# Performance work log

Measured on AMD Instinct MI355X. Metric: run time of the kernel, lower is better.

## Reference

```python
import jax, jax.numpy as jnp
import numpy as np
from math import sqrt

B, IN_C, OUT_C, H, W, WDIM, K = 16, 512, 512, 64, 64, 512, 3
EPS = 1e-8
LRELU_SLOPE = 0.2


def setup_inputs() -> dict:
    key = jax.random.key(0)
    ks = jax.random.split(key, 5)
    return {
        "x": jax.random.normal(ks[0], (B, IN_C, H, W), dtype=jnp.float32),
        "w": jax.random.normal(ks[1], (B, WDIM), dtype=jnp.float32),
        "noise": jax.random.normal(ks[2], (B, 1, H, W), dtype=jnp.float32),
        "linear_w": jax.random.normal(ks[3], (IN_C, WDIM), dtype=jnp.float32),
        "linear_b": jnp.ones((IN_C,), dtype=jnp.float32),
        "conv_w": jax.random.normal(ks[4], (OUT_C, IN_C, K, K), dtype=jnp.float32),
        "scale_noise": jnp.zeros((OUT_C,), dtype=jnp.float32),
        "bias": jnp.zeros((OUT_C,), dtype=jnp.float32),
    }


def reference(x, w, noise, linear_w, linear_b, conv_w, scale_noise, bias):
    # EqualizerStraights: equalized-lr linear, scale = 1/sqrt(w_dim)
    s = w @ (linear_w * (1.0 / sqrt(WDIM))).T + linear_b  # [b, in_c]
    # Weight_Demod: equalized conv weight, scale = 1/sqrt(in_c*k*k)
    base_w = conv_w * (1.0 / sqrt(IN_C * K * K))  # [out, in, k, k]
    weights = base_w[None] * s[:, None, :, None, None]  # [b, out, in, k, k]
    sigma_inv = jax.lax.rsqrt(
        jnp.sum(weights * weights, axis=(2, 3, 4), keepdims=True) + EPS)
    weights = weights * sigma_inv

    def conv1(xi, wi):  # xi [in,h,w], wi [out,in,k,k]
        return jax.lax.conv_general_dilated(
            xi[None], wi, window_strides=(1, 1), padding="SAME",
            dimension_numbers=("NCHW", "OIHW", "NCHW"))[0]

    y = jax.vmap(conv1)(x, weights)  # [b, out, h, w]
    y = y + scale_noise[None, :, None, None] * noise
    return jax.nn.leaky_relu(y + bias[None, :, None, None], negative_slope=LRELU_SLOPE)
```

## Files before the change

kernel.cpp:

```cpp
#include <hip/hip_runtime.h>
#include <hip/hip_bf16.h>
#include <stdint.h>

typedef __bf16 bf16_t;
typedef __bf16 bf16x8 __attribute__((ext_vector_type(8)));
typedef short short8 __attribute__((ext_vector_type(8)));
typedef float f32x4 __attribute__((ext_vector_type(4)));

#define RS512  0.044194173824159216f
#define RS4608 0.014731391274719739f

__global__ void k_style(const float* __restrict__ w, const float* __restrict__ lw,
                        const float* __restrict__ lb, float* __restrict__ s) {
  int b = blockIdx.y;
  int c = blockIdx.x * 256 + threadIdx.x;
  const float4* wr = (const float4*)(w + b * 512);
  const float4* lr = (const float4*)(lw + (size_t)c * 512);
  float acc = 0.f;
#pragma unroll 4
  for (int d = 0; d < 128; ++d) {
    float4 a = wr[d], q = lr[d];
    acc += a.x * q.x + a.y * q.y + a.z * q.z + a.w * q.w;
  }
  s[b * 512 + c] = acc * RS512 + lb[c];
}

__global__ void k_wprep(const float* __restrict__ cw, float* __restrict__ wsq,
                        bf16_t* __restrict__ bwf, f32x4* __restrict__ zb) {
  if (blockIdx.x == 0) zb[threadIdx.x] = (f32x4)0.f;
  int idx = blockIdx.x * 256 + threadIdx.x;
  int o = idx >> 9, i = idx & 511;
  float v[9];
  float ss = 0.f;
#pragma unroll
  for (int t = 0; t < 9; ++t) {
    float x = cw[(size_t)idx * 9 + t] * RS4608;
    v[t] = x;
    ss += x * x;
  }
  wsq[idx] = ss;
  int lane = (o & 15) | (((i >> 3) & 3) << 4);
  int base_blk = (i >> 5) * 32 + (o >> 4);
#pragma unroll
  for (int t = 0; t < 9; ++t) {
    size_t e = ((size_t)(t * 512 + base_blk) << 9) + lane * 8 + (i & 7);
    bwf[e] = (bf16_t)v[t];
  }
}

__global__ void k_sigma(const float* __restrict__ s, const float* __restrict__ wsq,
                        float* __restrict__ sinv) {
  __shared__ float s2[512];
  int b = blockIdx.y;
  int o = blockIdx.x * 256 + threadIdx.x;
  for (int i = threadIdx.x; i < 512; i += 256) {
    float v = s[b * 512 + i];
    s2[i] = v * v;
  }
  __syncthreads();
  const float4* qr = (const float4*)(wsq + (size_t)o * 512);
  float acc = 0.f;
#pragma unroll 4
  for (int d = 0; d < 128; ++d) {
    float4 q = qr[d];
    acc += q.x * s2[4 * d] + q.y * s2[4 * d + 1] + q.z * s2[4 * d + 2] + q.w * s2[4 * d + 3];
  }
  sinv[b * 512 + o] = rsqrtf(acc + 1e-8f);
}

__global__ void k_xt(const float* __restrict__ x, const float* __restrict__ s,
                     bf16_t* __restrict__ xt) {
  int ic = blockIdx.x, h = blockIdx.y, b = blockIdx.z;
  __shared__ __align__(16) bf16_t tile[8192];
  int t = threadIdx.x;
  int wcol = t & 63;
  int g = t >> 6;
#pragma unroll
  for (int blk = 0; blk < 4; ++blk) {
    int grp = blk * 4 + g;
    bf16x8 vec;
#pragma unroll
    for (int k = 0; k < 8; ++k) {
      int i = ic * 128 + grp * 8 + k;
      float v = x[(((size_t)b * 512 + i) * 64 + h) * 64 + wcol] * s[b * 512 + i];
      vec[k] = (bf16_t)v;
    }
    int chunk = grp ^ (wcol & 15);
    *(bf16x8*)((char*)tile + wcol * 256 + chunk * 16) = vec;
  }
  __syncthreads();
#pragma unroll
  for (int j = 0; j < 4; ++j) {
    int flat = j * 256 + t;
    int wo = flat >> 4, ig8 = flat & 15;
    int chunk = ig8 ^ (wo & 15);
    bf16x8 v = *(bf16x8*)((char*)tile + wo * 256 + chunk * 16);
    int c32 = (ig8 >> 2);
    int slot = (ig8 & 3) ^ ((wo >> 1) & 3);
    *(bf16x8*)(xt + (((size_t)b * 64 + h) * 64 + wo) * 512 + ic * 128 + c32 * 32 + slot * 8) = v;
  }
}

#define AS1 __attribute__((address_space(1)))
#define AS3 __attribute__((address_space(3)))

__device__ __forceinline__ void gl16(const void* g, void* l) {
  __builtin_amdgcn_global_load_lds((const AS1 void*)g, (AS3 void*)l, 16, 0, 0);
}

#define VMCNT(n) asm volatile("s_waitcnt vmcnt(" #n ")" ::: "memory")
#define BAR __builtin_amdgcn_s_barrier()

#define TMAP(jc) ((((jc) % 3) * 3) + ((jc) / 3))

__global__ __launch_bounds__(256, 2) void k_conv(
    const bf16_t* __restrict__ xt, const bf16_t* __restrict__ bwf,
    const float* __restrict__ sinv, const float* __restrict__ noise,
    const float* __restrict__ snz, const float* __restrict__ bias,
    const char* __restrict__ zb, float* __restrict__ out) {
  __shared__ __align__(16) char lds[73728];

  const int t = threadIdx.x;
  const int rq = blockIdx.x;
  const int OY = blockIdx.y;
  const int b = blockIdx.z;
  const int h0 = rq * 4;
  const int lane = t & 63;
  const int wv = t >> 6;
  const int wm = wv >> 1;
  const int wn = wv & 1;

  const char* xg = (const char*)xt + (size_t)b * 4194304 + (t >> 2) * 1024 + (t & 3) * 16;
  const char* wgp = (const char*)bwf + OY * 8192 + wv * 2048 + lane * 16;
  const char* zgv = zb + t * 16;

  f32x4 acc[4][8] = {};
  bf16x8 RA[4], RB[4];

  const uint32_t woff = (uint32_t)((wm << 12) + (lane << 4));
  uint32_t pX[4][3];
#pragma unroll
  for (int j = 0; j < 4; ++j)
#pragma unroll
    for (int dk = 0; dk < 3; ++dk) {
      int icol = j * 16 + (lane & 15) + dk - 1;
      int ic2 = icol < 0 ? 0 : (icol > 63 ? 63 : icol);
      int slot = (lane >> 4) ^ ((ic2 >> 1) & 3);
      pX[j][dk] = (uint32_t)(24576 + wn * 8192 + ic2 * 64 + slot * 16);
    }
  const bool c0 = (lane & 15) == 0;
  const bool c15 = (lane & 15) == 15;

  auto stW = [&](uint32_t srcByteOff, int slab) {
    const char* s0 = wgp + srcByteOff;
    gl16(s0, lds + slab * 8192 + (wv << 11));
    gl16(s0 + 1024, lds + slab * 8192 + (wv << 11) + 1024);
  };
  auto stX = [&](int r, uint32_t cxoff, int xb) {
    int gr = h0 - 1 + r;
    char* d = lds + 24576 + xb * 24576 + r * 4096 + (wv << 10);
    if ((unsigned)gr < 64u) gl16(xg + (size_t)gr * 65536 + cxoff, d);
    else gl16(zgv, d);
  };

#define LROW(DST, RREL, KX, XB)                                                \
  {                                                                            \
    _Pragma("unroll") for (int col = 0; col < 4; ++col) {                      \
      short8 xv = *(const short8*)(lds + pX[col][(KX)] +                       \
                                   (uint32_t)((XB) * 24576 + (RREL) * 4096));  \
      if ((KX) == 0 && col == 0) xv = c0 ? (short8)0 : xv;                     \
      if ((KX) == 2 && col == 3) xv = c15 ? (short8)0 : xv;                    \
      DST[col] = __builtin_bit_cast(bf16x8, xv);                               \
    }                                                                          \
  }

#define MFMABLK(LO, HI)                                                        \
  {                                                                            \
    __builtin_amdgcn_s_setprio(1);                                             \
    _Pragma("unroll") for (int mi = 0; mi < 4; ++mi) {                         \
      _Pragma("unroll") for (int col = 0; col < 4; ++col) {                    \
        acc[mi][col] = __builtin_amdgcn_mfma_f32_16x16x32_bf16(                \
            af[mi], LO[col], acc[mi][col], 0, 0, 0);                           \
        acc[mi][col + 4] = __builtin_amdgcn_mfma_f32_16x16x32_bf16(            \
            af[mi], HI[col], acc[mi][col + 4], 0, 0, 0);                       \
      }                                                                        \
    }                                                                          \
    __builtin_amdgcn_s_setprio(0);                                             \
  }

#define COMP(JC, XB)                                                           \
  {                                                                            \
    bf16x8 af[4];                                                              \
    _Pragma("unroll") for (int mi = 0; mi < 4; ++mi)                           \
        af[mi] = *(const bf16x8*)(lds + (uint32_t)(((JC) % 3) * 8192) + woff + \
                                  (uint32_t)(mi * 1024));                      \
    if ((JC) % 3 == 0) {                                                       \
      LROW(RA, 0, (JC) / 3, XB); LROW(RB, 1, (JC) / 3, XB);                    \
      MFMABLK(RA, RB);                                                         \
    } else if ((JC) % 3 == 1) {                                                \
      LROW(RA, 2, (JC) / 3, XB);                                               \
      MFMABLK(RB, RA);                                                         \
    } else {                                                                   \
      LROW(RB, 3, (JC) / 3, XB);                                               \
      MFMABLK(RA, RB);                                                         \
    }                                                                          \
  }

#define PHASE(CWB, CXB, JC, LAST, XB)                                          \
  {                                                                            \
    if (!(LAST) && (JC) < 6) stX((JC), (CXB), (XB) ^ 1);                       \
    if (!(LAST) || (JC) <= 6) {                                                \
      if ((JC) + 2 <= 8)                                                       \
        stW((CWB) + (uint32_t)(TMAP((JC) + 2)) * 524288u, ((JC) + 2) % 3);     \
      else                                                                     \
        stW((CWB) + 32768u + (uint32_t)(TMAP((JC) - 7)) * 524288u,             \
            ((JC) + 2) % 3);                                                   \
    }                                                                          \
    if (LAST) {                                                                \
      if ((JC) <= 6) { VMCNT(4); }                                             \
      else if ((JC) == 7) { VMCNT(2); }                                        \
      else { VMCNT(0); }                                                       \
    } else {                                                                   \
      if ((JC) == 0 || (JC) == 6) { VMCNT(5); }                                \
      else if ((JC) <= 5) { VMCNT(6); }                                        \
      else { VMCNT(4); }                                                       \
    }                                                                          \
    __builtin_amdgcn_s_barrier();                                              \
    COMP((JC), (XB));                                                          \
  }

#pragma unroll
  for (int r = 0; r < 6; ++r) stX(r, 0u, 0);
  stW(0u * 524288u, 0);
  stW(3u * 524288u, 1);
  VMCNT(0); BAR;

  uint32_t cwb = 0, cxb = 64;
#pragma unroll 1
  for (int ci = 0; ci < 7; ++ci) {
#pragma unroll
    for (int jc = 0; jc < 9; ++jc) PHASE(cwb, cxb, jc, 0, 0);
    cwb += 32768u; cxb += 64u;
#pragma unroll
    for (int jc = 0; jc < 9; ++jc) PHASE(cwb, cxb, jc, 0, 1);
    cwb += 32768u; cxb += 64u;
  }
#pragma unroll
  for (int jc = 0; jc < 9; ++jc) PHASE(cwb, cxb, jc, 0, 0);
  cwb += 32768u;
#pragma unroll
  for (int jc = 0; jc < 9; ++jc) PHASE(cwb, cxb, jc, 1, 1);

  const float* sb = sinv + b * 512;
  const int og = OY * 128 + wm * 64 + ((lane >> 4) << 2);
  const int colb = lane & 15;
  float nzv[8];
#pragma unroll
  for (int ni = 0; ni < 8; ++ni) {
    int prow = h0 + wn * 2 + (ni >> 2);
    nzv[ni] = noise[(size_t)b * 4096 + prow * 64 + (ni & 3) * 16 + colb];
  }
#pragma unroll
  for (int mi = 0; mi < 4; ++mi) {
#pragma unroll
    for (int r = 0; r < 4; ++r) {
      int o = og + mi * 16 + r;
      float sv = sb[o];
      float nw = snz[o];
      float bv = bias[o];
      float* obase = out + ((size_t)b * 512 + o) * 4096;
#pragma unroll
      for (int ni = 0; ni < 8; ++ni) {
        int prow = h0 + wn * 2 + (ni >> 2);
        int col = (ni & 3) * 16 + colb;
        float v = acc[mi][ni][r] * sv + nw * nzv[ni] + bv;
        obase[prow * 64 + col] = v > 0.f ? v : 0.2f * v;
      }
    }
  }
}

extern "C" void kernel_launch(void* const* d_in, const int* in_sizes, int n_in,
                              void* d_out, int out_size, void* d_ws, size_t ws_size,
                              hipStream_t stream) {
  const float* x     = (const float*)d_in[0];
  const float* w     = (const float*)d_in[1];
  const float* noise = (const float*)d_in[2];
  const float* lw    = (const float*)d_in[3];
  const float* lb    = (const float*)d_in[4];
  const float* cw    = (const float*)d_in[5];
  const float* snz   = (const float*)d_in[6];
  const float* bias  = (const float*)d_in[7];
  float* out = (float*)d_out;

  char* ws = (char*)d_ws;
  bf16_t* xt   = (bf16_t*)ws;
  bf16_t* bwf  = (bf16_t*)(ws + 67108864);
  float*  s    = (float*)(ws + 71827456);
  float*  sinv = (float*)(ws + 71860224);
  float*  wsq  = (float*)(ws + 71892992);
  char*   zbuf = ws + 72941568;

  k_style<<<dim3(2, 16), 256, 0, stream>>>(w, lw, lb, s);
  k_wprep<<<dim3(1024), 256, 0, stream>>>(cw, wsq, bwf, (f32x4*)zbuf);
  k_sigma<<<dim3(2, 16), 256, 0, stream>>>(s, wsq, sinv);
  k_xt<<<dim3(4, 64, 16), 256, 0, stream>>>(x, s, xt);
  k_conv<<<dim3(16, 4, 16), 256, 0, stream>>>(xt, bwf, sinv, noise, snz, bias, zbuf, out);
}
```

Baseline: 314.5 us.

## Split conv tile across eight waves with one output row per wave

The conv kernel moves from 256 to 512 threads per block. Each wave now owns one output row and half the accumulators (4x4 instead of 4x8 fragments), and the weight and input staging loads are redistributed across the eight waves. The tap ordering is simplified to ky-major, with the vmcnt wait counts and the LDS addressing rewritten to match. The aim is to lower register pressure and get more waves in flight to hide latency. The cost is more LDS fragment reads per MFMA and more barrier participants.

```diff
diff --git a/kernel.cpp b/kernel.cpp
--- a/kernel.cpp
+++ b/kernel.cpp
@@ -111,9 +111,7 @@
 #define VMCNT(n) asm volatile("s_waitcnt vmcnt(" #n ")" ::: "memory")
 #define BAR __builtin_amdgcn_s_barrier()
 
-#define TMAP(jc) ((((jc) % 3) * 3) + ((jc) / 3))
-
-__global__ __launch_bounds__(256, 2) void k_conv(
+__global__ __launch_bounds__(512, 4) void k_conv(
     const bf16_t* __restrict__ xt, const bf16_t* __restrict__ bwf,
     const float* __restrict__ sinv, const float* __restrict__ noise,
     const float* __restrict__ snz, const float* __restrict__ bias,
@@ -127,15 +125,24 @@
   const int h0 = rq * 4;
   const int lane = t & 63;
   const int wv = t >> 6;
-  const int wm = wv >> 1;
-  const int wn = wv & 1;
-
-  const char* xg = (const char*)xt + (size_t)b * 4194304 + (t >> 2) * 1024 + (t & 3) * 16;
-  const char* wgp = (const char*)bwf + OY * 8192 + wv * 2048 + lane * 16;
-  const char* zgv = zb + t * 16;
-
-  f32x4 acc[4][8] = {};
-  bf16x8 RA[4], RB[4];
+  const int wm = wv & 1;
+  const int wn = wv >> 1;
+
+  const char* xg = (const char*)xt + (size_t)b * 4194304 + (lane >> 2) * 1024 + (lane & 3) * 16;
+  const char* wgsrc = (const char*)bwf + ((OY * 8 + wv) << 10) + (lane << 4);
+
+  f32x4 acc[4][4] = {};
+
+  const char* xsrc[3];
+  uint32_t xdst[3];
+#pragma unroll
+  for (int k = 0; k < 3; ++k) {
+    int slot = wv * 3 + k, row = slot >> 2, q = slot & 3;
+    int gr = h0 - 1 + row;
+    bool valid = (unsigned)gr < 64u;
+    xsrc[k] = valid ? (xg + (size_t)gr * 65536 + q * 16384) : (zb + lane * 16);
+    xdst[k] = (uint32_t)(24576 + row * 4096 + q * 1024);
+  }
 
   const uint32_t woff = (uint32_t)((wm << 12) + (lane << 4));
   uint32_t pX[4][3];
@@ -146,93 +153,66 @@
       int icol = j * 16 + (lane & 15) + dk - 1;
       int ic2 = icol < 0 ? 0 : (icol > 63 ? 63 : icol);
       int slot = (lane >> 4) ^ ((ic2 >> 1) & 3);
-      pX[j][dk] = (uint32_t)(24576 + wn * 8192 + ic2 * 64 + slot * 16);
+      pX[j][dk] = (uint32_t)(24576 + wn * 4096 + ic2 * 64 + slot * 16);
     }
   const bool c0 = (lane & 15) == 0;
   const bool c15 = (lane & 15) == 15;
 
-  auto stW = [&](uint32_t srcByteOff, int slab) {
-    const char* s0 = wgp + srcByteOff;
-    gl16(s0, lds + slab * 8192 + (wv << 11));
-    gl16(s0 + 1024, lds + slab * 8192 + (wv << 11) + 1024);
+  auto stW = [&](uint32_t srcoff, int slab) {
+    gl16(wgsrc + srcoff, lds + slab * 8192 + (wv << 10));
   };
-  auto stX = [&](int r, uint32_t cxoff, int xb) {
-    int gr = h0 - 1 + r;
-    char* d = lds + 24576 + xb * 24576 + r * 4096 + (wv << 10);
-    if ((unsigned)gr < 64u) gl16(xg + (size_t)gr * 65536 + cxoff, d);
-    else gl16(zgv, d);
+  auto stX = [&](int k, uint32_t cxoff, int xb) {
+    gl16(xsrc[k] + cxoff, lds + xdst[k] + (uint32_t)(xb * 24576));
   };
 
-#define LROW(DST, RREL, KX, XB)                                                \
-  {                                                                            \
-    _Pragma("unroll") for (int col = 0; col < 4; ++col) {                      \
-      short8 xv = *(const short8*)(lds + pX[col][(KX)] +                       \
-                                   (uint32_t)((XB) * 24576 + (RREL) * 4096));  \
-      if ((KX) == 0 && col == 0) xv = c0 ? (short8)0 : xv;                     \
-      if ((KX) == 2 && col == 3) xv = c15 ? (short8)0 : xv;                    \
-      DST[col] = __builtin_bit_cast(bf16x8, xv);                               \
-    }                                                                          \
-  }
-
-#define MFMABLK(LO, HI)                                                        \
-  {                                                                            \
-    __builtin_amdgcn_s_setprio(1);                                             \
-    _Pragma("unroll") for (int mi = 0; mi < 4; ++mi) {                         \
-      _Pragma("unroll") for (int col = 0; col < 4; ++col) {                    \
-        acc[mi][col] = __builtin_amdgcn_mfma_f32_16x16x32_bf16(                \
-            af[mi], LO[col], acc[mi][col], 0, 0, 0);                           \
-        acc[mi][col + 4] = __builtin_amdgcn_mfma_f32_16x16x32_bf16(            \
-            af[mi], HI[col], acc[mi][col + 4], 0, 0, 0);                       \
-      }                                                                        \
-    }                                                                          \
-    __builtin_amdgcn_s_setprio(0);                                             \
-  }
-
-#define COMP(JC, XB)                                                           \
-  {                                                                            \
-    bf16x8 af[4];                                                              \
-    _Pragma("unroll") for (int mi = 0; mi < 4; ++mi)                           \
-        af[mi] = *(const bf16x8*)(lds + (uint32_t)(((JC) % 3) * 8192) + woff + \
-                                  (uint32_t)(mi * 1024));                      \
-    if ((JC) % 3 == 0) {                                                       \
-      LROW(RA, 0, (JC) / 3, XB); LROW(RB, 1, (JC) / 3, XB);                    \
-      MFMABLK(RA, RB);                                                         \
-    } else if ((JC) % 3 == 1) {                                                \
-      LROW(RA, 2, (JC) / 3, XB);                                               \
-      MFMABLK(RB, RA);                                                         \
-    } else {                                                                   \
-      LROW(RB, 3, (JC) / 3, XB);                                               \
-      MFMABLK(RA, RB);                                                         \
-    }                                                                          \
-  }
+  auto COMP = [&](int JC, int XB) {
+    const int ky = JC / 3, kx = JC % 3;
+    bf16x8 af[4];
+#pragma unroll
+    for (int mi = 0; mi < 4; ++mi)
+      af[mi] = *(const bf16x8*)(lds + (uint32_t)((JC % 3) * 8192) + woff + (uint32_t)(mi * 1024));
+    bf16x8 bfr[4];
+#pragma unroll
+    for (int col = 0; col < 4; ++col) {
+      short8 xv = *(const short8*)(lds + pX[col][kx] +
+                                   (uint32_t)(XB * 24576 + ky * 4096));
+      if (kx == 0 && col == 0) xv = c0 ? (short8)0 : xv;
+      if (kx == 2 && col == 3) xv = c15 ? (short8)0 : xv;
+      bfr[col] = __builtin_bit_cast(bf16x8, xv);
+    }
+    __builtin_amdgcn_s_setprio(1);
+#pragma unroll
+    for (int mi = 0; mi < 4; ++mi)
+#pragma unroll
+      for (int col = 0; col < 4; ++col)
+        acc[mi][col] =
+            __builtin_amdgcn_mfma_f32_16x16x32_bf16(af[mi], bfr[col], acc[mi][col], 0, 0, 0);
+    __builtin_amdgcn_s_setprio(0);
+  };
 
 #define PHASE(CWB, CXB, JC, LAST, XB)                                          \
   {                                                                            \
-    if (!(LAST) && (JC) < 6) stX((JC), (CXB), (XB) ^ 1);                       \
-    if (!(LAST) || (JC) <= 6) {                                                \
-      if ((JC) + 2 <= 8)                                                       \
-        stW((CWB) + (uint32_t)(TMAP((JC) + 2)) * 524288u, ((JC) + 2) % 3);     \
-      else                                                                     \
-        stW((CWB) + 32768u + (uint32_t)(TMAP((JC) - 7)) * 524288u,             \
-            ((JC) + 2) % 3);                                                   \
-    }                                                                          \
+    if ((JC) + 2 <= 8) stW((CWB) + (uint32_t)((JC) + 2) * 524288u, ((JC) + 2) % 3); \
+    else if (!(LAST)) stW((CWB) + 32768u + (uint32_t)((JC) - 7) * 524288u, ((JC) + 2) % 3); \
+    if (!(LAST) && (JC) < 3) stX((JC), (CXB), (XB) ^ 1);                       \
     if (LAST) {                                                                \
-      if ((JC) <= 6) { VMCNT(4); }                                             \
-      else if ((JC) == 7) { VMCNT(2); }                                        \
+      if ((JC) <= 6) { VMCNT(2); }                                             \
+      else if ((JC) == 7) { VMCNT(1); }                                        \
       else { VMCNT(0); }                                                       \
     } else {                                                                   \
-      if ((JC) == 0 || (JC) == 6) { VMCNT(5); }                                \
-      else if ((JC) <= 5) { VMCNT(6); }                                        \
-      else { VMCNT(4); }                                                       \
+      if ((JC) == 0 || (JC) == 4) { VMCNT(3); }                                \
+      else if ((JC) == 1 || (JC) == 3) { VMCNT(4); }                           \
+      else if ((JC) == 2) { VMCNT(5); }                                        \
+      else { VMCNT(2); }                                                       \
     }                                                                          \
     __builtin_amdgcn_s_barrier();                                              \
     COMP((JC), (XB));                                                          \
   }
 
 #pragma unroll
-  for (int r = 0; r < 6; ++r) stX(r, 0u, 0);
-  stW(0u * 524288u, 0);
-  stW(3u * 524288u, 1);
+  for (int k = 0; k < 3; ++k) stX(k, 0u, 0);
+  stW(0u, 0);
+  stW(524288u, 1);
   VMCNT(0); BAR;
 
   uint32_t cwb = 0, cxb = 64;
@@ -249,17 +229,16 @@
   for (int jc = 0; jc < 9; ++jc) PHASE(cwb, cxb, jc, 0, 0);
   cwb += 32768u;
 #pragma unroll
-  for (int jc = 0; jc < 9; ++jc) PHASE(cwb, cxb, jc, 1, 1);
+  for (int jc = 0; jc < 9; ++jc) PHASE(cwb, 0u, jc, 1, 1);
 
   const float* sb = sinv + b * 512;
   const int og = OY * 128 + wm * 64 + ((lane >> 4) << 2);
   const int colb = lane & 15;
-  float nzv[8];
-#pragma unroll
-  for (int ni = 0; ni < 8; ++ni) {
-    int prow = h0 + wn * 2 + (ni >> 2);
-    nzv[ni] = noise[(size_t)b * 4096 + prow * 64 + (ni & 3) * 16 + colb];
-  }
+  const int prow = h0 + wn;
+  float nzv[4];
+#pragma unroll
+  for (int col = 0; col < 4; ++col)
+    nzv[col] = noise[(size_t)b * 4096 + prow * 64 + col * 16 + colb];
 #pragma unroll
   for (int mi = 0; mi < 4; ++mi) {
 #pragma unroll
@@ -268,13 +247,11 @@
       float sv = sb[o];
       float nw = snz[o];
       float bv = bias[o];
-      float* obase = out + ((size_t)b * 512 + o) * 4096;
-#pragma unroll
-      for (int ni = 0; ni < 8; ++ni) {
-        int prow = h0 + wn * 2 + (ni >> 2);
-        int col = (ni & 3) * 16 + colb;
-        float v = acc[mi][ni][r] * sv + nw * nzv[ni] + bv;
-        obase[prow * 64 + col] = v > 0.f ? v : 0.2f * v;
+      float* orow = out + (((size_t)b * 512 + o) * 64 + prow) * 64;
+#pragma unroll
+      for (int col = 0; col < 4; ++col) {
+        float v = acc[mi][col][r] * sv + nw * nzv[col] + bv;
+        orow[col * 16 + colb] = v > 0.f ? v : 0.2f * v;
       }
     }
   }
@@ -305,5 +282,5 @@
   k_wprep<<<dim3(1024), 256, 0, stream>>>(cw, wsq, bwf, (f32x4*)zbuf);
   k_sigma<<<dim3(2, 16), 256, 0, stream>>>(s, wsq, sinv);
   k_xt<<<dim3(4, 64, 16), 256, 0, stream>>>(x, s, xt);
-  k_conv<<<dim3(16, 4, 16), 256, 0, stream>>>(xt, bwf, sinv, noise, snz, bias, zbuf, out);
-}
+  k_conv<<<dim3(16, 4, 16), 512, 0, stream>>>(xt, bwf, sinv, noise, snz, bias, zbuf, out);
+}
```

Result: faster. 302.8 us (-3.7%).
